# Kernel optimization log

Measured on AMD Instinct MI355X. Metric: run time of the kernel, lower is better.

Reference implementation:

```python
import jax, jax.numpy as jnp
import numpy as np

N, F, T, H, E, OUT, HEADS = 20000, 32, 12, 64, 320000, 12, 2


def setup_inputs() -> dict:
    key = jax.random.key(0)
    ks = iter(jax.random.split(key, 40))

    def nrm(shape, scale):
        return jax.random.normal(next(ks), shape, jnp.float32) * scale

    g0 = 2 * H + F   # gate input dim, cell 0
    g1 = 2 * H + H   # gate input dim, cell 1
    inp = {
        "x": nrm((N, F, T), 1.0),
        "edge_index": jax.random.randint(next(ks), (2, E), 0, N, dtype=jnp.int32),
        "edge_attr": jax.random.uniform(next(ks), (E, 2), dtype=jnp.float32),
        # cell 0: GCNConv + GRU gates (weights stored [in, out])
        "Wg0": nrm((F, H), F ** -0.5), "bg0": nrm((H,), 0.02),
        "Wu0": nrm((g0, H), g0 ** -0.5), "bu0": nrm((H,), 0.02),
        "Wr0": nrm((g0, H), g0 ** -0.5), "br0": nrm((H,), 0.02),
        "Wc0": nrm((g0, H), g0 ** -0.5), "bc0": nrm((H,), 0.02),
        # cell 1
        "Wg1": nrm((H, H), H ** -0.5), "bg1": nrm((H,), 0.02),
        "Wu1": nrm((g1, H), g1 ** -0.5), "bu1": nrm((H,), 0.02),
        "Wr1": nrm((g1, H), g1 ** -0.5), "br1": nrm((H,), 0.02),
        "Wc1": nrm((g1, H), g1 ** -0.5), "bc1": nrm((H,), 0.02),
        # temporal multi-head attention (torch layout: [out, in])
        "in_proj_w": nrm((3 * H, H), H ** -0.5), "in_proj_b": nrm((3 * H,), 0.02),
        "out_proj_w": nrm((H, H), H ** -0.5), "out_proj_b": nrm((H,), 0.02),
        # output head ([in, out])
        "out_w": nrm((H, OUT), H ** -0.5), "out_b": nrm((OUT,), 0.02),
    }
    return inp


def reference(x, edge_index, edge_attr,
              Wg0, bg0, Wu0, bu0, Wr0, br0, Wc0, bc0,
              Wg1, bg1, Wu1, bu1, Wr1, br1, Wc1, bc1,
              in_proj_w, in_proj_b, out_proj_w, out_proj_b,
              out_w, out_b):
    n, f, t = x.shape
    h_dim = Wg0.shape[1]
    src, dst = edge_index[0], edge_index[1]
    w = edge_attr[:, -1]

    # GCN normalization with self-loops (PyG gcn_norm)
    loop = jnp.arange(n)
    src_all = jnp.concatenate([src, loop])
    dst_all = jnp.concatenate([dst, loop])
    w_all = jnp.concatenate([w, jnp.ones((n,), x.dtype)])
    deg = jax.ops.segment_sum(w_all, dst_all, num_segments=n)
    dinv = jnp.where(deg > 0, jax.lax.rsqrt(deg), 0.0)
    norm = dinv[src_all] * w_all * dinv[dst_all]  # [E+N]

    def gcn(xi, W, b):
        xw = xi @ W  # [N, H]
        msg = norm[:, None] * xw[src_all]  # gather from sources
        return jax.ops.segment_sum(msg, dst_all, num_segments=n) + b

    def cell(xi, h, W, b, Wu, bu, Wr, br, Wc, bc):
        g = jax.nn.sigmoid(gcn(xi, W, b))
        zu = jnp.concatenate([xi, g, h], axis=-1)
        u = jax.nn.sigmoid(zu @ Wu + bu)
        r = jax.nn.sigmoid(zu @ Wr + br)
        zc = jnp.concatenate([xi, g, r * h], axis=-1)
        c = jnp.tanh(zc @ Wc + bc)
        return u * h + (1.0 - u) * c

    def step(carry, x_t):
        h0, h1 = carry
        h0 = cell(x_t, h0, Wg0, bg0, Wu0, bu0, Wr0, br0, Wc0, bc0)
        h1 = cell(h0, h1, Wg1, bg1, Wu1, bu1, Wr1, br1, Wc1, bc1)
        return (h0, h1), h1

    x_seq = jnp.transpose(x, (2, 0, 1))  # [T, N, F]
    h0 = jnp.zeros((n, h_dim), x.dtype)
    _, h_seq = jax.lax.scan(step, (h0, h0), x_seq)  # [T, N, H] (== [S, B, H])

    # temporal multi-head self-attention per node
    heads = HEADS
    dh = h_dim // heads
    qkv = h_seq @ in_proj_w.T + in_proj_b  # [T, N, 3H]
    q, k, v = jnp.split(qkv, 3, axis=-1)

    def split_heads(a):
        return jnp.transpose(a.reshape(t, n, heads, dh), (1, 2, 0, 3))  # [N, h, T, dh]

    q, k, v = split_heads(q), split_heads(k), split_heads(v)
    scores = jnp.einsum('nhtd,nhsd->nhts', q, k) / jnp.sqrt(jnp.asarray(dh, x.dtype))
    attn = jax.nn.softmax(scores, axis=-1)
    o = jnp.einsum('nhts,nhsd->nhtd', attn, v)
    o = jnp.transpose(o, (2, 0, 1, 3)).reshape(t, n, h_dim)
    o = o @ out_proj_w.T + out_proj_b  # [T, N, H]

    h_attn = o.mean(axis=0)  # agg='mean' over sequence -> [N, H]
    return h_attn @ out_w + out_b  # [N, OUT]
```

## Files before the change

kernel.cpp:

```cpp
#include <hip/hip_runtime.h>
#include <math.h>

#define NN 20000
#define FF 32
#define TT 12
#define HH 64
#define EE 320000
#define OUTD 12
#define CB1 1250
#define GB  2500
#define HST 832
#define QS  196

typedef __attribute__((ext_vector_type(8))) short short8;
typedef __attribute__((ext_vector_type(4))) float floatx4;

__device__ __forceinline__ float aexp2(float x) {
    float r; asm("v_exp_f32 %0, %1" : "=v"(r) : "v"(x)); return r;
}
__device__ __forceinline__ float arcp(float x) {
    float r; asm("v_rcp_f32 %0, %1" : "=v"(r) : "v"(x)); return r;
}
#define LOG2E 1.44269504088896f
__device__ __forceinline__ float fsig(float x) { return arcp(1.f + aexp2(-LOG2E * x)); }
__device__ __forceinline__ float ftanh(float x) {
    return fmaf(-2.f, arcp(1.f + aexp2(2.f * LOG2E * x)), 1.f);
}

__device__ __forceinline__ unsigned short bf16rne(float f) {
    union { float f; unsigned u; } v; v.f = f;
    unsigned u = v.u;
    u += 0x7fffu + ((u >> 16) & 1u);
    return (unsigned short)(u >> 16);
}
__device__ __forceinline__ float lof(unsigned v) {
    union { unsigned u; float f; } x; x.u = v << 16; return x.f;
}
__device__ __forceinline__ float hif(unsigned v) {
    union { unsigned u; float f; } x; x.u = v & 0xffff0000u; return x.f;
}
__device__ __forceinline__ unsigned packbf(float a, float b) {
    return (unsigned)bf16rne(a) | ((unsigned)bf16rne(b) << 16);
}

#define MFMA(a, b, c) __builtin_amdgcn_mfma_f32_16x16x32_bf16((a), (b), (c), 0, 0, 0)


__global__ void init_all(float* deg, int* cnt, unsigned* h0s2u, unsigned* hseqTu) {
    int i = blockIdx.x * 256 + threadIdx.x;
    if (i < NN) { deg[i] = 1.0f; cnt[i] = 0; }
    if (i < NN * HH / 2) { h0s2u[i] = 0u; }
    if (i < NN * 32) { hseqTu[(size_t)(i >> 5) * (HST / 2) + (i & 31)] = 0u; }
}

__global__ void edge_accum_kernel(const int* ei, const float* ea, float* deg, int* cnt) {
    int e = blockIdx.x * 256 + threadIdx.x;
    if (e >= EE) return;
    int d = ei[EE + e];
    float w = ea[e * 2 + 1];
    atomicAdd(&deg[d], w);
    atomicAdd(&cnt[d], 1);
}

__global__ void scan_dinv(const int* cnt, int* rowptr, int* cursor,
                          const float* deg, float* dinv) {
    if (blockIdx.x != 0) {
        int i = (blockIdx.x - 1) * 1024 + threadIdx.x;
        if (i < NN) dinv[i] = rsqrtf(deg[i]);
        return;
    }
    __shared__ int wsum[16];
    int tid = threadIdx.x;
    int lane = tid & 63, w = tid >> 6;
    int run = 0;
    for (int base = 0; base < NN; base += 1024) {
        int idx = base + tid;
        int c = (idx < NN) ? cnt[idx] : 0;
        int v = c;
        #pragma unroll
        for (int off = 1; off < 64; off <<= 1) {
            int t = __shfl_up(v, off, 64);
            if (lane >= off) v += t;
        }
        if (lane == 63) wsum[w] = v;
        __syncthreads();
        if (tid < 16) {
            int x = wsum[tid];
            #pragma unroll
            for (int off = 1; off < 16; off <<= 1) {
                int t = __shfl_up(x, off, 64);
                if (tid >= off) x += t;
            }
            wsum[tid] = x;
        }
        __syncthreads();
        int waveoff = (w > 0) ? wsum[w - 1] : 0;
        int excl = run + waveoff + (v - c);
        if (idx < NN) { rowptr[idx] = excl; cursor[idx] = excl; }
        run += wsum[15];
        __syncthreads();
    }
    if (tid == 0) rowptr[NN] = run;
}

__global__ void fill_kernel(const int* ei, const float* ea, const float* dinv,
                            int* cursor, int2* colval) {
    int e = blockIdx.x * 256 + threadIdx.x;
    if (e >= EE) return;
    int s = ei[e], d = ei[EE + e];
    float w = ea[e * 2 + 1];
    int pos = atomicAdd(&cursor[d], 1);
    colval[pos] = make_int2(s, __float_as_int(dinv[s] * w * dinv[d]));
}

#define TPB 1250
#define WCB 336
__global__ void prep_misc(const float* __restrict__ x, unsigned short* __restrict__ xTs,
                          const float* Wg0, const float* Wu0, const float* Wr0, const float* Wc0,
                          const float* Wg1, const float* Wu1, const float* Wr1, const float* Wc1,
                          const float* ipw,
                          short* Wg0T, short* Wu0T, short* Wr0T, short* Wc0T,
                          short* Wg1T, short* Wu1T, short* Wr1T, short* Wc1T, short* ipwB,
                          const float* opw, const float* opb, const float* ow, const float* ob,
                          float* OW2, float* ob2) {
    int b = blockIdx.x;
    if (b < TPB) {
        __shared__ float tl[16 * 416];
        int n0 = b * 16;
        const float* xb = x + (size_t)n0 * 384;
        int tid = threadIdx.x;
        #pragma unroll
        for (int k = 0; k < 24; ++k) {
            int i = tid + 256 * k;
            float v = xb[i];
            int nn = i / 384;
            int rem = i - nn * 384;
            int f = rem / 12;
            int t2 = rem - f * 12;
            tl[nn * 416 + f * 13 + t2] = v;
        }
        __syncthreads();
        #pragma unroll
        for (int k = 0; k < 24; ++k) {
            int o = tid + 256 * k;
            int f = o & 31;
            int nn = (o >> 5) & 15;
            int t = o >> 9;
            xTs[(size_t)t * (NN * FF) + (size_t)(n0 + nn) * 32 + f] =
                bf16rne(tl[nn * 416 + f * 13 + t]);
        }
        return;
    }
    if (b < TPB + WCB) {
        int i = (b - TPB) * 256 + threadIdx.x;
        if (i < 2048) { int n = i / 32, k = i % 32; Wg0T[i] = (short)bf16rne(Wg0[k * 64 + n]); return; }
        i -= 2048;
        if (i < 10240) { int n = i / 160, k = i % 160; Wu0T[i] = (short)bf16rne(Wu0[k * 64 + n]); return; }
        i -= 10240;
        if (i < 10240) { int n = i / 160, k = i % 160; Wr0T[i] = (short)bf16rne(Wr0[k * 64 + n]); return; }
        i -= 10240;
        if (i < 10240) { int n = i / 160, k = i % 160; Wc0T[i] = (short)bf16rne(Wc0[k * 64 + n]); return; }
        i -= 10240;
        if (i < 4096) { int n = i / 64, k = i % 64; Wg1T[i] = (short)bf16rne(Wg1[k * 64 + n]); return; }
        i -= 4096;
        if (i < 12288) { int n = i / 192, k = i % 192; Wu1T[i] = (short)bf16rne(Wu1[k * 64 + n]); return; }
        i -= 12288;
        if (i < 12288) { int n = i / 192, k = i % 192; Wr1T[i] = (short)bf16rne(Wr1[k * 64 + n]); return; }
        i -= 12288;
        if (i < 12288) { int n = i / 192, k = i % 192; Wc1T[i] = (short)bf16rne(Wc1[k * 64 + n]); return; }
        i -= 12288;
        if (i < 12288) { ipwB[i] = (short)bf16rne(ipw[i]); }
        return;
    }
    {
        int i = (b - TPB - WCB) * 256 + threadIdx.x;
        if (i < 64 * OUTD) {
            int k = i / OUTD, d = i - k * OUTD;
            float acc = 0.f;
            for (int j = 0; j < 64; ++j) acc += opw[j * 64 + k] * ow[j * OUTD + d];
            OW2[i] = acc;
        } else if (i < 64 * OUTD + OUTD) {
            int d = i - 64 * OUTD;
            float acc = ob[d];
            for (int j = 0; j < 64; ++j) acc += opb[j] * ow[j * OUTD + d];
            ob2[d] = acc;
        }
    }
}

__global__ void gather_raw32(const unsigned short* __restrict__ xTs, const float* __restrict__ dinv,
                             const int* __restrict__ rowptr, const int2* __restrict__ colval,
                             unsigned short* __restrict__ aggxs) {
    const unsigned* src = (const unsigned*)(xTs + (size_t)blockIdx.y * NN * 32);
    unsigned* dst = (unsigned*)(aggxs + (size_t)blockIdx.y * NN * 32);
    int node = blockIdx.x * 16 + (threadIdx.x >> 4);
    int l2 = threadIdx.x & 15;
    float di = dinv[node];
    float dd = di * di;
    unsigned v = src[node * 16 + l2];
    float a0 = dd * lof(v), a1 = dd * hif(v);
    int s = rowptr[node], e = rowptr[node + 1];
    int j = s;
    for (; j + 7 < e; j += 8) {
        int2 c[8];
        #pragma unroll
        for (int q = 0; q < 8; ++q) c[q] = colval[j + q];
        unsigned vv[8];
        #pragma unroll
        for (int q = 0; q < 8; ++q) vv[q] = src[c[q].x * 16 + l2];
        #pragma unroll
        for (int q = 0; q < 8; ++q) {
            float w = __int_as_float(c[q].y);
            a0 += w * lof(vv[q]); a1 += w * hif(vv[q]);
        }
    }
    for (; j + 3 < e; j += 4) {
        int2 cv0 = colval[j], cv1 = colval[j + 1], cv2 = colval[j + 2], cv3 = colval[j + 3];
        float w0 = __int_as_float(cv0.y), w1 = __int_as_float(cv1.y);
        float w2 = __int_as_float(cv2.y), w3 = __int_as_float(cv3.y);
        unsigned v0 = src[cv0.x * 16 + l2], v1 = src[cv1.x * 16 + l2];
        unsigned v2 = src[cv2.x * 16 + l2], v3 = src[cv3.x * 16 + l2];
        a0 += w0 * lof(v0) + w1 * lof(v1) + w2 * lof(v2) + w3 * lof(v3);
        a1 += w0 * hif(v0) + w1 * hif(v1) + w2 * hif(v2) + w3 * hif(v3);
    }
    for (; j < e; ++j) {
        int2 cv = colval[j];
        unsigned vv = src[cv.x * 16 + l2];
        float w = __int_as_float(cv.y);
        a0 += w * lof(vv); a1 += w * hif(vv);
    }
    dst[node * 16 + l2] = packbf(a0, a1);
}

__device__ __forceinline__ void gather_g1_body(
    int blk, const unsigned short* __restrict__ y0s, const float* __restrict__ dinv,
    const int* __restrict__ rowptr, const int2* __restrict__ colval,
    const float* __restrict__ bg1, unsigned short* __restrict__ g1s) {
    const unsigned* yp = (const unsigned*)y0s;
    int node = blk * 8 + (threadIdx.x >> 5);
    int l2 = threadIdx.x & 31;
    float di = dinv[node];
    float dd = di * di;
    unsigned v = yp[node * 32 + l2];
    float a0 = dd * lof(v), a1 = dd * hif(v);
    int s = rowptr[node], e = rowptr[node + 1];
    int j = s;
    for (; j + 7 < e; j += 8) {
        int2 c[8];
        #pragma unroll
        for (int q = 0; q < 8; ++q) c[q] = colval[j + q];
        unsigned vv[8];
        #pragma unroll
        for (int q = 0; q < 8; ++q) vv[q] = yp[c[q].x * 32 + l2];
        #pragma unroll
        for (int q = 0; q < 8; ++q) {
            float w = __int_as_float(c[q].y);
            a0 += w * lof(vv[q]); a1 += w * hif(vv[q]);
        }
    }
    for (; j + 3 < e; j += 4) {
        int2 cv0 = colval[j], cv1 = colval[j + 1], cv2 = colval[j + 2], cv3 = colval[j + 3];
        float w0 = __int_as_float(cv0.y), w1 = __int_as_float(cv1.y);
        float w2 = __int_as_float(cv2.y), w3 = __int_as_float(cv3.y);
        unsigned v0 = yp[cv0.x * 32 + l2], v1 = yp[cv1.x * 32 + l2];
        unsigned v2 = yp[cv2.x * 32 + l2], v3 = yp[cv3.x * 32 + l2];
        a0 += w0 * lof(v0) + w1 * lof(v1) + w2 * lof(v2) + w3 * lof(v3);
        a1 += w0 * hif(v0) + w1 * hif(v1) + w2 * hif(v2) + w3 * hif(v3);
    }
    for (; j < e; ++j) {
        int2 cv = colval[j];
        unsigned vv = yp[cv.x * 32 + l2];
        float w = __int_as_float(cv.y);
        a0 += w * lof(vv); a1 += w * hif(vv);
    }
    float g0v = fsig(a0 + bg1[2 * l2]);
    float g1v = fsig(a1 + bg1[2 * l2 + 1]);
    ((unsigned*)g1s)[node * 32 + l2] = packbf(g0v, g1v);
}


__launch_bounds__(256, 4)
__global__ void mfma_g0(const unsigned short* __restrict__ aggxs, const short* __restrict__ Wg0T,
                        const float* __restrict__ bg0, unsigned short* __restrict__ g0s) {
    int tid = threadIdx.x;
    int wv = tid >> 6, lane = tid & 63;
    int quad = lane >> 4, ln = lane & 15;
    int m0 = blockIdx.x * 64 + wv * 16;
    short8 af = *reinterpret_cast<const short8*>(aggxs + (size_t)(m0 + ln) * 32 + quad * 8);
    floatx4 z = {0.f, 0.f, 0.f, 0.f};
    floatx4 acc[4] = {z, z, z, z};
    #pragma unroll
    for (int ct = 0; ct < 4; ++ct) {
        short8 bf = *reinterpret_cast<const short8*>(Wg0T + (size_t)(ct * 16 + ln) * 32 + quad * 8);
        acc[ct] = MFMA(af, bf, acc[ct]);
    }
    #pragma unroll
    for (int ct = 0; ct < 4; ++ct) {
        int col = ct * 16 + ln;
        float bb = bg0[col];
        #pragma unroll
        for (int r = 0; r < 4; ++r) {
            int row = m0 + quad * 4 + r;
            g0s[(size_t)row * 64 + col] = bf16rne(fsig(acc[ct][r] + bb));
        }
    }
}


__device__ __forceinline__ void cell0_body(
    int m0, short* T,
    const unsigned short* __restrict__ xt, const unsigned short* __restrict__ g0,
    const unsigned short* __restrict__ h0s,
    const short* __restrict__ Wu0T, const short* __restrict__ Wr0T,
    const short* __restrict__ Wc0T, const short* __restrict__ Wg1T,
    const float* __restrict__ bu0, const float* __restrict__ br0,
    const float* __restrict__ bc0,
    unsigned short* __restrict__ h0ns, unsigned short* __restrict__ y0s) {
    int tid = threadIdx.x;
    int wv = tid >> 6, lane = tid & 63;
    int quad = lane >> 4, ln = lane & 15;
    int arow = m0 + ln;
    int col = wv * 16 + ln;

    short8 af[5];
    af[0] = *reinterpret_cast<const short8*>(xt + (size_t)arow * 32 + quad * 8);
    af[1] = *reinterpret_cast<const short8*>(g0 + (size_t)arow * 64 + quad * 8);
    af[2] = *reinterpret_cast<const short8*>(g0 + (size_t)arow * 64 + 32 + quad * 8);
    af[3] = *reinterpret_cast<const short8*>(h0s + (size_t)arow * 64 + quad * 8);
    af[4] = *reinterpret_cast<const short8*>(h0s + (size_t)arow * 64 + 32 + quad * 8);

    floatx4 z = {0.f, 0.f, 0.f, 0.f};
    floatx4 aU = z, aR = z;
    const short* bu = Wu0T + (size_t)col * 160;
    const short* br = Wr0T + (size_t)col * 160;
    #pragma unroll
    for (int kc = 0; kc < 5; ++kc) {
        int ko = kc * 32 + quad * 8;
        aU = MFMA(af[kc], *reinterpret_cast<const short8*>(bu + ko), aU);
        aR = MFMA(af[kc], *reinterpret_cast<const short8*>(br + ko), aR);
    }
    float bU = bu0[col], bR = br0[col];
    float uu[4], hv[4];
    #pragma unroll
    for (int r = 0; r < 4; ++r) {
        int grow = m0 + quad * 4 + r;
        uu[r] = fsig(aU[r] + bU);
        hv[r] = lof((unsigned)h0s[(size_t)grow * 64 + col]);
        float rh = fsig(aR[r] + bR) * hv[r];
        T[(quad * 4 + r) * 72 + col] = (short)bf16rne(rh);
    }
    __syncthreads();

    short8 ar0 = *reinterpret_cast<const short8*>(T + ln * 72 + quad * 8);
    short8 ar1 = *reinterpret_cast<const short8*>(T + ln * 72 + 32 + quad * 8);
    floatx4 aC = z;
    const short* bc = Wc0T + (size_t)col * 160;
    #pragma unroll
    for (int kc = 0; kc < 3; ++kc)
        aC = MFMA(af[kc], *reinterpret_cast<const short8*>(bc + kc * 32 + quad * 8), aC);
    aC = MFMA(ar0, *reinterpret_cast<const short8*>(bc + 96 + quad * 8), aC);
    aC = MFMA(ar1, *reinterpret_cast<const short8*>(bc + 128 + quad * 8), aC);
    __syncthreads();

    float bC = bc0[col];
    #pragma unroll
    for (int r = 0; r < 4; ++r) {
        int grow = m0 + quad * 4 + r;
        float cv = ftanh(aC[r] + bC);
        float hn = uu[r] * hv[r] + (1.f - uu[r]) * cv;
        unsigned short hb = bf16rne(hn);
        h0ns[(size_t)grow * 64 + col] = hb;
        T[(quad * 4 + r) * 72 + col] = (short)hb;
    }
    __syncthreads();

    short8 ah0 = *reinterpret_cast<const short8*>(T + ln * 72 + quad * 8);
    short8 ah1 = *reinterpret_cast<const short8*>(T + ln * 72 + 32 + quad * 8);
    floatx4 aY = z;
    const short* bg = Wg1T + (size_t)col * 64;
    aY = MFMA(ah0, *reinterpret_cast<const short8*>(bg + quad * 8), aY);
    aY = MFMA(ah1, *reinterpret_cast<const short8*>(bg + 32 + quad * 8), aY);
    #pragma unroll
    for (int r = 0; r < 4; ++r) {
        int grow = m0 + quad * 4 + r;
        y0s[(size_t)grow * 64 + col] = bf16rne(aY[r]);
    }
}

__device__ __forceinline__ void cell1_body(
    int m0, short* T,
    const unsigned short* __restrict__ h0s, const unsigned short* __restrict__ g1s,
    const unsigned short* __restrict__ h1sT_in,
    const short* __restrict__ Wu1T, const short* __restrict__ Wr1T,
    const short* __restrict__ Wc1T,
    const float* __restrict__ bu1, const float* __restrict__ br1,
    const float* __restrict__ bc1,
    unsigned short* __restrict__ h1sT_out) {
    int tid = threadIdx.x;
    int wv = tid >> 6, lane = tid & 63;
    int quad = lane >> 4, ln = lane & 15;
    int arow = m0 + ln;
    int col = wv * 16 + ln;

    short8 af[6];
    af[0] = *reinterpret_cast<const short8*>(h0s + (size_t)arow * 64 + quad * 8);
    af[1] = *reinterpret_cast<const short8*>(h0s + (size_t)arow * 64 + 32 + quad * 8);
    af[2] = *reinterpret_cast<const short8*>(g1s + (size_t)arow * 64 + quad * 8);
    af[3] = *reinterpret_cast<const short8*>(g1s + (size_t)arow * 64 + 32 + quad * 8);
    af[4] = *reinterpret_cast<const short8*>(h1sT_in + (size_t)arow * HST + quad * 8);
    af[5] = *reinterpret_cast<const short8*>(h1sT_in + (size_t)arow * HST + 32 + quad * 8);

    floatx4 z = {0.f, 0.f, 0.f, 0.f};
    floatx4 aU = z, aR = z;
    const short* bu = Wu1T + (size_t)col * 192;
    const short* br = Wr1T + (size_t)col * 192;
    #pragma unroll
    for (int kc = 0; kc < 6; ++kc) {
        int ko = kc * 32 + quad * 8;
        aU = MFMA(af[kc], *reinterpret_cast<const short8*>(bu + ko), aU);
        aR = MFMA(af[kc], *reinterpret_cast<const short8*>(br + ko), aR);
    }
    float bU = bu1[col], bR = br1[col];
    float uu[4], hv[4];
    #pragma unroll
    for (int r = 0; r < 4; ++r) {
        int grow = m0 + quad * 4 + r;
        uu[r] = fsig(aU[r] + bU);
        hv[r] = lof((unsigned)h1sT_in[(size_t)grow * HST + col]);
        float rh = fsig(aR[r] + bR) * hv[r];
        T[(quad * 4 + r) * 72 + col] = (short)bf16rne(rh);
    }
    __syncthreads();

    short8 ar0 = *reinterpret_cast<const short8*>(T + ln * 72 + quad * 8);
    short8 ar1 = *reinterpret_cast<const short8*>(T + ln * 72 + 32 + quad * 8);
    floatx4 aC = z;
    const short* bc = Wc1T + (size_t)col * 192;
    #pragma unroll
    for (int kc = 0; kc < 4; ++kc)
        aC = MFMA(af[kc], *reinterpret_cast<const short8*>(bc + kc * 32 + quad * 8), aC);
    aC = MFMA(ar0, *reinterpret_cast<const short8*>(bc + 128 + quad * 8), aC);
    aC = MFMA(ar1, *reinterpret_cast<const short8*>(bc + 160 + quad * 8), aC);

    float bC = bc1[col];
    #pragma unroll
    for (int r = 0; r < 4; ++r) {
        int grow = m0 + quad * 4 + r;
        float cv = ftanh(aC[r] + bC);
        float hn = uu[r] * hv[r] + (1.f - uu[r]) * cv;
        h1sT_out[(size_t)grow * HST + col] = bf16rne(hn);
    }
}


struct PipeArgs {
    const float* dinv; const int* rowptr; const int2* colval;
    const short* Wu0T; const short* Wr0T; const short* Wc0T; const short* Wg1T;
    const float* bu0; const float* br0; const float* bc0;
    const short* Wu1T; const short* Wr1T; const short* Wc1T;
    const float* bu1; const float* br1; const float* bc1; const float* bg1;
    int c0n;
    const unsigned short* c0_xt; const unsigned short* c0_g0;
    const unsigned short* c0_hs_in;
    unsigned short* c0_hs_out; unsigned short* c0_y0_out;
    int gn;
    const unsigned short* g_y0; unsigned short* g_g1;
    int c1n;
    const unsigned short* c1_h0s; const unsigned short* c1_g1;
    const unsigned short* c1_hsT_in;
    unsigned short* c1_hsT_out;
};

__launch_bounds__(256, 6)
__global__ void pipe_step(PipeArgs A) {
    __shared__ short T[16 * 72];
    int b = blockIdx.x;
    if (b < A.c0n) {
        cell0_body(b * 16, T, A.c0_xt, A.c0_g0, A.c0_hs_in,
                   A.Wu0T, A.Wr0T, A.Wc0T, A.Wg1T, A.bu0, A.br0, A.bc0,
                   A.c0_hs_out, A.c0_y0_out);
        return;
    }
    b -= A.c0n;
    if (b < A.gn) {
        gather_g1_body(b, A.g_y0, A.dinv, A.rowptr, A.colval, A.bg1, A.g_g1);
        return;
    }
    b -= A.gn;
    cell1_body(b * 16, T, A.c1_h0s, A.c1_g1, A.c1_hsT_in,
               A.Wu1T, A.Wr1T, A.Wc1T, A.bu1, A.br1, A.bc1,
               A.c1_hsT_out);
}

__launch_bounds__(256, 6)
__global__ void attn_fused(const unsigned short* __restrict__ hseqT,
                           const short* __restrict__ ipwB, const float* __restrict__ ipb,
                           const float* __restrict__ OW2, const float* __restrict__ ob2,
                           float* __restrict__ out) {
    __shared__ __align__(16) unsigned short qtile[4][16 * QS];
    __shared__ float fbuf[4][64];
    __shared__ float wbuf[4][32];
    int wv = threadIdx.x >> 6, lane = threadIdx.x & 63;
    int node = blockIdx.x * 4 + wv;
    int quad = lane >> 4, ln = lane & 15;
    unsigned short* q = qtile[wv];
    float* sob = fbuf[wv];
    float* W = wbuf[wv];

    short8 zero8 = {0, 0, 0, 0, 0, 0, 0, 0};
    short8 af0 = zero8, af1 = zero8;
    if (ln < TT) {
        const unsigned short* hp = hseqT + (size_t)node * HST + (size_t)(ln + 1) * 64;
        af0 = *reinterpret_cast<const short8*>(hp + quad * 8);
        af1 = *reinterpret_cast<const short8*>(hp + 32 + quad * 8);
    }
    floatx4 z = {0.f, 0.f, 0.f, 0.f};
    #pragma unroll
    for (int ct = 0; ct < 12; ++ct) {
        const short* br = ipwB + (size_t)(ct * 16 + ln) * 64;
        floatx4 acc = MFMA(af0, *reinterpret_cast<const short8*>(br + quad * 8), z);
        acc = MFMA(af1, *reinterpret_cast<const short8*>(br + 32 + quad * 8), acc);
        int col = ct * 16 + ln;
        float bb = ipb[col];
        #pragma unroll
        for (int r = 0; r < 4; ++r)
            q[(quad * 4 + r) * QS + col] = bf16rne(acc[r] + bb);
    }
    __threadfence_block();

    floatx4 sc[2];
    #pragma unroll
    for (int h = 0; h < 2; ++h) {
        short8 aQ = *reinterpret_cast<const short8*>(q + ln * QS + h * 32 + quad * 8);
        short8 bK = *reinterpret_cast<const short8*>(q + ln * QS + 64 + h * 32 + quad * 8);
        sc[h] = MFMA(aQ, bK, z);
    }
    const float scl = 0.17677669529663687f;
    bool colok = ln < 12;
    #pragma unroll
    for (int h = 0; h < 2; ++h) {
        float p[4];
        #pragma unroll
        for (int r = 0; r < 4; ++r) {
            float e = colok ? aexp2(LOG2E * scl * sc[h][r]) : 0.f;
            float s = e;
            s += __shfl_xor(s, 1, 64);
            s += __shfl_xor(s, 2, 64);
            s += __shfl_xor(s, 4, 64);
            s += __shfl_xor(s, 8, 64);
            p[r] = e * arcp(s);
        }
        float ts = (quad < 3) ? (p[0] + p[1] + p[2] + p[3]) : 0.f;
        ts += __shfl_xor(ts, 16, 64);
        ts += __shfl_xor(ts, 32, 64);
        if (quad == 0) W[h * 16 + ln] = ts * (1.f / 12.f);
    }
    __threadfence_block();

    {
        int d = lane, hd = d >> 5, dd = d & 31;
        float acc = 0.f;
        #pragma unroll
        for (int ts = 0; ts < 12; ++ts)
            acc += W[hd * 16 + ts] * lof((unsigned)q[ts * QS + 128 + hd * 32 + dd]);
        sob[d] = acc;
    }
    __threadfence_block();

    {
        float acc = 0.f;
        if (ln < OUTD) {
            int k0 = quad * 16;
            #pragma unroll
            for (int k = 0; k < 16; ++k)
                acc = fmaf(sob[k0 + k], OW2[(k0 + k) * OUTD + ln], acc);
        }
        acc += __shfl_xor(acc, 16, 64);
        acc += __shfl_xor(acc, 32, 64);
        if (quad == 0 && ln < OUTD)
            out[(size_t)node * OUTD + ln] = acc + ob2[ln];
    }
}


extern "C" void kernel_launch(void* const* d_in, const int* in_sizes, int n_in,
                              void* d_out, int out_size, void* d_ws, size_t ws_size,
                              hipStream_t stream) {
    const float* x   = (const float*)d_in[0];
    const int*   ei  = (const int*)d_in[1];
    const float* ea  = (const float*)d_in[2];
    const float* Wg0 = (const float*)d_in[3];
    const float* bg0 = (const float*)d_in[4];
    const float* Wu0 = (const float*)d_in[5];
    const float* bu0 = (const float*)d_in[6];
    const float* Wr0 = (const float*)d_in[7];
    const float* br0 = (const float*)d_in[8];
    const float* Wc0 = (const float*)d_in[9];
    const float* bc0 = (const float*)d_in[10];
    const float* Wg1 = (const float*)d_in[11];
    const float* bg1 = (const float*)d_in[12];
    const float* Wu1 = (const float*)d_in[13];
    const float* bu1 = (const float*)d_in[14];
    const float* Wr1 = (const float*)d_in[15];
    const float* br1 = (const float*)d_in[16];
    const float* Wc1 = (const float*)d_in[17];
    const float* bc1 = (const float*)d_in[18];
    const float* ipw = (const float*)d_in[19];
    const float* ipb = (const float*)d_in[20];
    const float* opw = (const float*)d_in[21];
    const float* opb = (const float*)d_in[22];
    const float* ow  = (const float*)d_in[23];
    const float* ob  = (const float*)d_in[24];
    float* out = (float*)d_out;

    char* p = (char*)d_ws;
    auto alloc = [&](size_t bytes) { char* r = p; p += (bytes + 255) & ~(size_t)255; return (void*)r; };
    unsigned short* hseqT = (unsigned short*)alloc((size_t)NN * HST * 2);
    short* Wg0T = (short*)alloc((size_t)64 * 32 * 2);
    short* Wu0T = (short*)alloc((size_t)64 * 160 * 2);
    short* Wr0T = (short*)alloc((size_t)64 * 160 * 2);
    short* Wc0T = (short*)alloc((size_t)64 * 160 * 2);
    short* Wg1T = (short*)alloc((size_t)64 * 64 * 2);
    short* Wu1T = (short*)alloc((size_t)64 * 192 * 2);
    short* Wr1T = (short*)alloc((size_t)64 * 192 * 2);
    short* Wc1T = (short*)alloc((size_t)64 * 192 * 2);
    short* ipwB = (short*)alloc((size_t)192 * 64 * 2);
    float* OW2  = (float*)alloc((size_t)64 * OUTD * 4);
    float* ob2  = (float*)alloc((size_t)OUTD * 4);
    float* dinv   = (float*)alloc((size_t)NN * 4);
    int*   rowptr = (int*)  alloc((size_t)(NN + 1) * 4);
    int2*  colval = (int2*) alloc((size_t)EE * 8);
    unsigned short* xTs   = (unsigned short*)alloc((size_t)TT * NN * FF * 2);
    unsigned short* aggxs = (unsigned short*)alloc((size_t)TT * NN * FF * 2);
    unsigned short* g0s   = (unsigned short*)alloc((size_t)TT * NN * HH * 2);
    float* deg    = (float*)alloc((size_t)NN * 4);
    int*   cnt    = (int*)  alloc((size_t)NN * 4);
    int*   cursor = (int*)  alloc((size_t)NN * 4);
    unsigned short* y0sA = (unsigned short*)alloc((size_t)NN * HH * 2);
    unsigned short* y0sB = (unsigned short*)alloc((size_t)NN * HH * 2);
    unsigned short* g1sA = (unsigned short*)alloc((size_t)NN * HH * 2);
    unsigned short* g1sB = (unsigned short*)alloc((size_t)NN * HH * 2);
    unsigned short* h0s0 = (unsigned short*)alloc((size_t)NN * HH * 2);
    unsigned short* h0s1 = (unsigned short*)alloc((size_t)NN * HH * 2);
    unsigned short* h0s2 = (unsigned short*)alloc((size_t)NN * HH * 2);
    (void)ws_size;

    init_all<<<(NN * HH + 255) / 256, 256, 0, stream>>>(
        deg, cnt, (unsigned*)h0s2, (unsigned*)hseqT);
    edge_accum_kernel<<<(EE + 255) / 256, 256, 0, stream>>>(ei, ea, deg, cnt);
    scan_dinv<<<1 + (NN + 1023) / 1024, 1024, 0, stream>>>(cnt, rowptr, cursor, deg, dinv);
    fill_kernel<<<(EE + 255) / 256, 256, 0, stream>>>(ei, ea, dinv, cursor, colval);
    prep_misc<<<TPB + WCB + 4, 256, 0, stream>>>(
        x, xTs,
        Wg0, Wu0, Wr0, Wc0, Wg1, Wu1, Wr1, Wc1, ipw,
        Wg0T, Wu0T, Wr0T, Wc0T, Wg1T, Wu1T, Wr1T, Wc1T, ipwB,
        opw, opb, ow, ob, OW2, ob2);

    gather_raw32<<<dim3(NN / 16, TT), 256, 0, stream>>>(xTs, dinv, rowptr, colval, aggxs);
    mfma_g0<<<(TT * NN) / 64, 256, 0, stream>>>(aggxs, Wg0T, bg0, g0s);

    unsigned short* h0sB[3] = {h0s0, h0s1, h0s2};
    unsigned short* y0B[2] = {y0sA, y0sB};
    unsigned short* g1B[2] = {g1sA, g1sB};

    PipeArgs base;
    base.dinv = dinv; base.rowptr = rowptr; base.colval = colval;
    base.Wu0T = Wu0T; base.Wr0T = Wr0T; base.Wc0T = Wc0T; base.Wg1T = Wg1T;
    base.bu0 = bu0; base.br0 = br0; base.bc0 = bc0;
    base.Wu1T = Wu1T; base.Wr1T = Wr1T; base.Wc1T = Wc1T;
    base.bu1 = bu1; base.br1 = br1; base.bc1 = bc1; base.bg1 = bg1;

    for (int l = 0; l <= TT + 1; ++l) {
        PipeArgs A = base;
        int tc0 = l, tg = l - 1, tc1 = l - 2;

        A.c0n = (tc0 < TT) ? CB1 : 0;
        if (A.c0n) {
            A.c0_xt = xTs + (size_t)tc0 * NN * FF;
            A.c0_g0 = g0s + (size_t)tc0 * NN * HH;
            A.c0_hs_in = h0sB[(tc0 + 2) % 3];
            A.c0_hs_out = h0sB[tc0 % 3];
            A.c0_y0_out = y0B[tc0 & 1];
        } else {
            A.c0_xt = xTs; A.c0_g0 = g0s; A.c0_hs_in = h0sB[0];
            A.c0_hs_out = h0sB[0]; A.c0_y0_out = y0B[0];
        }

        A.gn = (tg >= 0 && tg < TT) ? GB : 0;
        if (A.gn) { A.g_y0 = y0B[tg & 1]; A.g_g1 = g1B[tg & 1]; }
        else { A.g_y0 = y0B[0]; A.g_g1 = g1B[0]; }

        A.c1n = (tc1 >= 0 && tc1 < TT) ? CB1 : 0;
        if (A.c1n) {
            A.c1_h0s = h0sB[tc1 % 3];
            A.c1_g1 = g1B[tc1 & 1];
            A.c1_hsT_in = hseqT + (size_t)tc1 * 64;
            A.c1_hsT_out = hseqT + (size_t)(tc1 + 1) * 64;
        } else {
            A.c1_h0s = h0sB[0]; A.c1_g1 = g1B[0];
            A.c1_hsT_in = hseqT; A.c1_hsT_out = hseqT;
        }

        int grid = A.c0n + A.gn + A.c1n;
        pipe_step<<<grid, 256, 0, stream>>>(A);
    }

    attn_fused<<<NN / 4, 256, 0, stream>>>(hseqT, ipwB, ipb, OW2, ob2, out);
}
```

Baseline: 756.4 us.

## Process 32 rows per GRU cell block and interleave block roles in pipe step

```diff
diff --git a/kernel.cpp b/kernel.cpp
--- a/kernel.cpp
+++ b/kernel.cpp
@@ -7,7 +7,7 @@
 #define HH 64
 #define EE 320000
 #define OUTD 12
-#define CB1 1250
+#define CT2 625
 #define GB  2500
 #define HST 832
 #define QS  196
@@ -319,71 +319,104 @@
     int tid = threadIdx.x;
     int wv = tid >> 6, lane = tid & 63;
     int quad = lane >> 4, ln = lane & 15;
-    int arow = m0 + ln;
     int col = wv * 16 + ln;
-
-    short8 af[5];
-    af[0] = *reinterpret_cast<const short8*>(xt + (size_t)arow * 32 + quad * 8);
-    af[1] = *reinterpret_cast<const short8*>(g0 + (size_t)arow * 64 + quad * 8);
-    af[2] = *reinterpret_cast<const short8*>(g0 + (size_t)arow * 64 + 32 + quad * 8);
-    af[3] = *reinterpret_cast<const short8*>(h0s + (size_t)arow * 64 + quad * 8);
-    af[4] = *reinterpret_cast<const short8*>(h0s + (size_t)arow * 64 + 32 + quad * 8);
+    int a0r = m0 + ln, a1r = m0 + 16 + ln;
+
+    short8 af0[5], af1[5];
+    af0[0] = *reinterpret_cast<const short8*>(xt + (size_t)a0r * 32 + quad * 8);
+    af1[0] = *reinterpret_cast<const short8*>(xt + (size_t)a1r * 32 + quad * 8);
+    af0[1] = *reinterpret_cast<const short8*>(g0 + (size_t)a0r * 64 + quad * 8);
+    af1[1] = *reinterpret_cast<const short8*>(g0 + (size_t)a1r * 64 + quad * 8);
+    af0[2] = *reinterpret_cast<const short8*>(g0 + (size_t)a0r * 64 + 32 + quad * 8);
+    af1[2] = *reinterpret_cast<const short8*>(g0 + (size_t)a1r * 64 + 32 + quad * 8);
+    af0[3] = *reinterpret_cast<const short8*>(h0s + (size_t)a0r * 64 + quad * 8);
+    af1[3] = *reinterpret_cast<const short8*>(h0s + (size_t)a1r * 64 + quad * 8);
+    af0[4] = *reinterpret_cast<const short8*>(h0s + (size_t)a0r * 64 + 32 + quad * 8);
+    af1[4] = *reinterpret_cast<const short8*>(h0s + (size_t)a1r * 64 + 32 + quad * 8);
 
     floatx4 z = {0.f, 0.f, 0.f, 0.f};
-    floatx4 aU = z, aR = z;
+    floatx4 aU0 = z, aR0 = z, aU1 = z, aR1 = z;
     const short* bu = Wu0T + (size_t)col * 160;
     const short* br = Wr0T + (size_t)col * 160;
     #pragma unroll
     for (int kc = 0; kc < 5; ++kc) {
         int ko = kc * 32 + quad * 8;
-        aU = MFMA(af[kc], *reinterpret_cast<const short8*>(bu + ko), aU);
-        aR = MFMA(af[kc], *reinterpret_cast<const short8*>(br + ko), aR);
+        short8 wu = *reinterpret_cast<const short8*>(bu + ko);
+        short8 wr = *reinterpret_cast<const short8*>(br + ko);
+        aU0 = MFMA(af0[kc], wu, aU0);
+        aU1 = MFMA(af1[kc], wu, aU1);
+        aR0 = MFMA(af0[kc], wr, aR0);
+        aR1 = MFMA(af1[kc], wr, aR1);
     }
     float bU = bu0[col], bR = br0[col];
-    float uu[4], hv[4];
+    float uu0[4], hv0[4], uu1[4], hv1[4];
     #pragma unroll
     for (int r = 0; r < 4; ++r) {
-        int grow = m0 + quad * 4 + r;
-        uu[r] = fsig(aU[r] + bU);
-        hv[r] = lof((unsigned)h0s[(size_t)grow * 64 + col]);
-        float rh = fsig(aR[r] + bR) * hv[r];
-        T[(quad * 4 + r) * 72 + col] = (short)bf16rne(rh);
+        int g0r = m0 + quad * 4 + r, g1r = m0 + 16 + quad * 4 + r;
+        uu0[r] = fsig(aU0[r] + bU);
+        uu1[r] = fsig(aU1[r] + bU);
+        hv0[r] = lof((unsigned)h0s[(size_t)g0r * 64 + col]);
+        hv1[r] = lof((unsigned)h0s[(size_t)g1r * 64 + col]);
+        T[(quad * 4 + r) * 72 + col] = (short)bf16rne(fsig(aR0[r] + bR) * hv0[r]);
+        T[(16 + quad * 4 + r) * 72 + col] = (short)bf16rne(fsig(aR1[r] + bR) * hv1[r]);
     }
     __syncthreads();
 
-    short8 ar0 = *reinterpret_cast<const short8*>(T + ln * 72 + quad * 8);
-    short8 ar1 = *reinterpret_cast<const short8*>(T + ln * 72 + 32 + quad * 8);
-    floatx4 aC = z;
+    short8 p00 = *reinterpret_cast<const short8*>(T + ln * 72 + quad * 8);
+    short8 p01 = *reinterpret_cast<const short8*>(T + ln * 72 + 32 + quad * 8);
+    short8 p10 = *reinterpret_cast<const short8*>(T + (16 + ln) * 72 + quad * 8);
+    short8 p11 = *reinterpret_cast<const short8*>(T + (16 + ln) * 72 + 32 + quad * 8);
+    floatx4 aC0 = z, aC1 = z;
     const short* bc = Wc0T + (size_t)col * 160;
     #pragma unroll
-    for (int kc = 0; kc < 3; ++kc)
-        aC = MFMA(af[kc], *reinterpret_cast<const short8*>(bc + kc * 32 + quad * 8), aC);
-    aC = MFMA(ar0, *reinterpret_cast<const short8*>(bc + 96 + quad * 8), aC);
-    aC = MFMA(ar1, *reinterpret_cast<const short8*>(bc + 128 + quad * 8), aC);
+    for (int kc = 0; kc < 3; ++kc) {
+        short8 wc = *reinterpret_cast<const short8*>(bc + kc * 32 + quad * 8);
+        aC0 = MFMA(af0[kc], wc, aC0);
+        aC1 = MFMA(af1[kc], wc, aC1);
+    }
+    {
+        short8 wc3 = *reinterpret_cast<const short8*>(bc + 96 + quad * 8);
+        short8 wc4 = *reinterpret_cast<const short8*>(bc + 128 + quad * 8);
+        aC0 = MFMA(p00, wc3, aC0);
+        aC1 = MFMA(p10, wc3, aC1);
+        aC0 = MFMA(p01, wc4, aC0);
+        aC1 = MFMA(p11, wc4, aC1);
+    }
     __syncthreads();
 
     float bC = bc0[col];
     #pragma unroll
     for (int r = 0; r < 4; ++r) {
-        int grow = m0 + quad * 4 + r;
-        float cv = ftanh(aC[r] + bC);
-        float hn = uu[r] * hv[r] + (1.f - uu[r]) * cv;
-        unsigned short hb = bf16rne(hn);
-        h0ns[(size_t)grow * 64 + col] = hb;
-        T[(quad * 4 + r) * 72 + col] = (short)hb;
+        int g0r = m0 + quad * 4 + r, g1r = m0 + 16 + quad * 4 + r;
+        float hn0 = uu0[r] * hv0[r] + (1.f - uu0[r]) * ftanh(aC0[r] + bC);
+        float hn1 = uu1[r] * hv1[r] + (1.f - uu1[r]) * ftanh(aC1[r] + bC);
+        unsigned short hb0 = bf16rne(hn0), hb1 = bf16rne(hn1);
+        h0ns[(size_t)g0r * 64 + col] = hb0;
+        h0ns[(size_t)g1r * 64 + col] = hb1;
+        T[(quad * 4 + r) * 72 + col] = (short)hb0;
+        T[(16 + quad * 4 + r) * 72 + col] = (short)hb1;
     }
     __syncthreads();
 
-    short8 ah0 = *reinterpret_cast<const short8*>(T + ln * 72 + quad * 8);
-    short8 ah1 = *reinterpret_cast<const short8*>(T + ln * 72 + 32 + quad * 8);
-    floatx4 aY = z;
+    short8 h00 = *reinterpret_cast<const short8*>(T + ln * 72 + quad * 8);
+    short8 h01 = *reinterpret_cast<const short8*>(T + ln * 72 + 32 + quad * 8);
+    short8 h10 = *reinterpret_cast<const short8*>(T + (16 + ln) * 72 + quad * 8);
+    short8 h11 = *reinterpret_cast<const short8*>(T + (16 + ln) * 72 + 32 + quad * 8);
+    floatx4 aY0 = z, aY1 = z;
     const short* bg = Wg1T + (size_t)col * 64;
-    aY = MFMA(ah0, *reinterpret_cast<const short8*>(bg + quad * 8), aY);
-    aY = MFMA(ah1, *reinterpret_cast<const short8*>(bg + 32 + quad * 8), aY);
+    {
+        short8 w0 = *reinterpret_cast<const short8*>(bg + quad * 8);
+        short8 w1 = *reinterpret_cast<const short8*>(bg + 32 + quad * 8);
+        aY0 = MFMA(h00, w0, aY0);
+        aY1 = MFMA(h10, w0, aY1);
+        aY0 = MFMA(h01, w1, aY0);
+        aY1 = MFMA(h11, w1, aY1);
+    }
     #pragma unroll
     for (int r = 0; r < 4; ++r) {
-        int grow = m0 + quad * 4 + r;
-        y0s[(size_t)grow * 64 + col] = bf16rne(aY[r]);
+        int g0r = m0 + quad * 4 + r, g1r = m0 + 16 + quad * 4 + r;
+        y0s[(size_t)g0r * 64 + col] = bf16rne(aY0[r]);
+        y0s[(size_t)g1r * 64 + col] = bf16rne(aY1[r]);
     }
 }
 
@@ -399,56 +432,80 @@
     int tid = threadIdx.x;
     int wv = tid >> 6, lane = tid & 63;
     int quad = lane >> 4, ln = lane & 15;
-    int arow = m0 + ln;
     int col = wv * 16 + ln;
-
-    short8 af[6];
-    af[0] = *reinterpret_cast<const short8*>(h0s + (size_t)arow * 64 + quad * 8);
-    af[1] = *reinterpret_cast<const short8*>(h0s + (size_t)arow * 64 + 32 + quad * 8);
-    af[2] = *reinterpret_cast<const short8*>(g1s + (size_t)arow * 64 + quad * 8);
-    af[3] = *reinterpret_cast<const short8*>(g1s + (size_t)arow * 64 + 32 + quad * 8);
-    af[4] = *reinterpret_cast<const short8*>(h1sT_in + (size_t)arow * HST + quad * 8);
-    af[5] = *reinterpret_cast<const short8*>(h1sT_in + (size_t)arow * HST + 32 + quad * 8);
+    int a0r = m0 + ln, a1r = m0 + 16 + ln;
+
+    short8 af0[6], af1[6];
+    af0[0] = *reinterpret_cast<const short8*>(h0s + (size_t)a0r * 64 + quad * 8);
+    af1[0] = *reinterpret_cast<const short8*>(h0s + (size_t)a1r * 64 + quad * 8);
+    af0[1] = *reinterpret_cast<const short8*>(h0s + (size_t)a0r * 64 + 32 + quad * 8);
+    af1[1] = *reinterpret_cast<const short8*>(h0s + (size_t)a1r * 64 + 32 + quad * 8);
+    af0[2] = *reinterpret_cast<const short8*>(g1s + (size_t)a0r * 64 + quad * 8);
+    af1[2] = *reinterpret_cast<const short8*>(g1s + (size_t)a1r * 64 + quad * 8);
+    af0[3] = *reinterpret_cast<const short8*>(g1s + (size_t)a0r * 64 + 32 + quad * 8);
+    af1[3] = *reinterpret_cast<const short8*>(g1s + (size_t)a1r * 64 + 32 + quad * 8);
+    af0[4] = *reinterpret_cast<const short8*>(h1sT_in + (size_t)a0r * HST + quad * 8);
+    af1[4] = *reinterpret_cast<const short8*>(h1sT_in + (size_t)a1r * HST + quad * 8);
+    af0[5] = *reinterpret_cast<const short8*>(h1sT_in + (size_t)a0r * HST + 32 + quad * 8);
+    af1[5] = *reinterpret_cast<const short8*>(h1sT_in + (size_t)a1r * HST + 32 + quad * 8);
 
     floatx4 z = {0.f, 0.f, 0.f, 0.f};
-    floatx4 aU = z, aR = z;
+    floatx4 aU0 = z, aR0 = z, aU1 = z, aR1 = z;
     const short* bu = Wu1T + (size_t)col * 192;
     const short* br = Wr1T + (size_t)col * 192;
     #pragma unroll
     for (int kc = 0; kc < 6; ++kc) {
         int ko = kc * 32 + quad * 8;
-        aU = MFMA(af[kc], *reinterpret_cast<const short8*>(bu + ko), aU);
-        aR = MFMA(af[kc], *reinterpret_cast<const short8*>(br + ko), aR);
+        short8 wu = *reinterpret_cast<const short8*>(bu + ko);
+        short8 wr = *reinterpret_cast<const short8*>(br + ko);
+        aU0 = MFMA(af0[kc], wu, aU0);
+        aU1 = MFMA(af1[kc], wu, aU1);
+        aR0 = MFMA(af0[kc], wr, aR0);
+        aR1 = MFMA(af1[kc], wr, aR1);
     }
     float bU = bu1[col], bR = br1[col];
-    float uu[4], hv[4];
+    float uu0[4], hv0[4], uu1[4], hv1[4];
     #pragma unroll
     for (int r = 0; r < 4; ++r) {
-        int grow = m0 + quad * 4 + r;
-        uu[r] = fsig(aU[r] + bU);
-        hv[r] = lof((unsigned)h1sT_in[(size_t)grow * HST + col]);
-        float rh = fsig(aR[r] + bR) * hv[r];
-        T[(quad * 4 + r) * 72 + col] = (short)bf16rne(rh);
+        int g0r = m0 + quad * 4 + r, g1r = m0 + 16 + quad * 4 + r;
+        uu0[r] = fsig(aU0[r] + bU);
+        uu1[r] = fsig(aU1[r] + bU);
+        hv0[r] = lof((unsigned)h1sT_in[(size_t)g0r * HST + col]);
+        hv1[r] = lof((unsigned)h1sT_in[(size_t)g1r * HST + col]);
+        T[(quad * 4 + r) * 72 + col] = (short)bf16rne(fsig(aR0[r] + bR) * hv0[r]);
+        T[(16 + quad * 4 + r) * 72 + col] = (short)bf16rne(fsig(aR1[r] + bR) * hv1[r]);
     }
     __syncthreads();
 
-    short8 ar0 = *reinterpret_cast<const short8*>(T + ln * 72 + quad * 8);
-    short8 ar1 = *reinterpret_cast<const short8*>(T + ln * 72 + 32 + quad * 8);
-    floatx4 aC = z;
+    short8 p00 = *reinterpret_cast<const short8*>(T + ln * 72 + quad * 8);
+    short8 p01 = *reinterpret_cast<const short8*>(T + ln * 72 + 32 + quad * 8);
+    short8 p10 = *reinterpret_cast<const short8*>(T + (16 + ln) * 72 + quad * 8);
+    short8 p11 = *reinterpret_cast<const short8*>(T + (16 + ln) * 72 + 32 + quad * 8);
+    floatx4 aC0 = z, aC1 = z;
     const short* bc = Wc1T + (size_t)col * 192;
     #pragma unroll
-    for (int kc = 0; kc < 4; ++kc)
-        aC = MFMA(af[kc], *reinterpret_cast<const short8*>(bc + kc * 32 + quad * 8), aC);
-    aC = MFMA(ar0, *reinterpret_cast<const short8*>(bc + 128 + quad * 8), aC);
-    aC = MFMA(ar1, *reinterpret_cast<const short8*>(bc + 160 + quad * 8), aC);
+    for (int kc = 0; kc < 4; ++kc) {
+        short8 wc = *reinterpret_cast<const short8*>(bc + kc * 32 + quad * 8);
+        aC0 = MFMA(af0[kc], wc, aC0);
+        aC1 = MFMA(af1[kc], wc, aC1);
+    }
+    {
+        short8 wc4 = *reinterpret_cast<const short8*>(bc + 128 + quad * 8);
+        short8 wc5 = *reinterpret_cast<const short8*>(bc + 160 + quad * 8);
+        aC0 = MFMA(p00, wc4, aC0);
+        aC1 = MFMA(p10, wc4, aC1);
+        aC0 = MFMA(p01, wc5, aC0);
+        aC1 = MFMA(p11, wc5, aC1);
+    }
 
     float bC = bc1[col];
     #pragma unroll
     for (int r = 0; r < 4; ++r) {
-        int grow = m0 + quad * 4 + r;
-        float cv = ftanh(aC[r] + bC);
-        float hn = uu[r] * hv[r] + (1.f - uu[r]) * cv;
-        h1sT_out[(size_t)grow * HST + col] = bf16rne(hn);
+        int g0r = m0 + quad * 4 + r, g1r = m0 + 16 + quad * 4 + r;
+        float hn0 = uu0[r] * hv0[r] + (1.f - uu0[r]) * ftanh(aC0[r] + bC);
+        float hn1 = uu1[r] * hv1[r] + (1.f - uu1[r]) * ftanh(aC1[r] + bC);
+        h1sT_out[(size_t)g0r * HST + col] = bf16rne(hn0);
+        h1sT_out[(size_t)g1r * HST + col] = bf16rne(hn1);
     }
 }
 
@@ -473,21 +530,22 @@
 
 __launch_bounds__(256, 6)
 __global__ void pipe_step(PipeArgs A) {
-    __shared__ short T[16 * 72];
-    int b = blockIdx.x;
-    if (b < A.c0n) {
-        cell0_body(b * 16, T, A.c0_xt, A.c0_g0, A.c0_hs_in,
+    __shared__ short T[32 * 72];
+    int per = (A.c0n ? 1 : 0) + (A.gn ? 4 : 0) + (A.c1n ? 1 : 0);
+    int q = blockIdx.x / per;
+    int r = blockIdx.x - q * per;
+    int goff = A.c0n ? 1 : 0;
+    if (A.c0n && r == 0) {
+        cell0_body(q * 32, T, A.c0_xt, A.c0_g0, A.c0_hs_in,
                    A.Wu0T, A.Wr0T, A.Wc0T, A.Wg1T, A.bu0, A.br0, A.bc0,
                    A.c0_hs_out, A.c0_y0_out);
         return;
     }
-    b -= A.c0n;
-    if (b < A.gn) {
-        gather_g1_body(b, A.g_y0, A.dinv, A.rowptr, A.colval, A.bg1, A.g_g1);
+    if (A.gn && r >= goff && r < goff + 4) {
+        gather_g1_body(q * 4 + (r - goff), A.g_y0, A.dinv, A.rowptr, A.colval, A.bg1, A.g_g1);
         return;
     }
-    b -= A.gn;
-    cell1_body(b * 16, T, A.c1_h0s, A.c1_g1, A.c1_hsT_in,
+    cell1_body(q * 32, T, A.c1_h0s, A.c1_g1, A.c1_hsT_in,
                A.Wu1T, A.Wr1T, A.Wc1T, A.bu1, A.br1, A.bc1,
                A.c1_hsT_out);
 }
@@ -674,7 +732,7 @@
         PipeArgs A = base;
         int tc0 = l, tg = l - 1, tc1 = l - 2;
 
-        A.c0n = (tc0 < TT) ? CB1 : 0;
+        A.c0n = (tc0 < TT) ? CT2 : 0;
         if (A.c0n) {
             A.c0_xt = xTs + (size_t)tc0 * NN * FF;
             A.c0_g0 = g0s + (size_t)tc0 * NN * HH;
@@ -690,7 +748,7 @@
         if (A.gn) { A.g_y0 = y0B[tg & 1]; A.g_g1 = g1B[tg & 1]; }
         else { A.g_y0 = y0B[0]; A.g_g1 = g1B[0]; }
 
-        A.c1n = (tc1 >= 0 && tc1 < TT) ? CB1 : 0;
+        A.c1n = (tc1 >= 0 && tc1 < TT) ? CT2 : 0;
         if (A.c1n) {
             A.c1_h0s = h0sB[tc1 % 3];
             A.c1_g1 = g1B[tc1 & 1];
```

Measured after the change: 702.9 us (median of 2 runs). 1.08x faster.
